# Kernel tuning notes

Measured on AMD Instinct MI355X. Metric: run time of the kernel, lower is better.

## Reference

```python
import jax, jax.numpy as jnp
import numpy as np

D_MODEL = 1024
NUM_HEADS = 16
D_K = D_MODEL // NUM_HEADS
B, L = 2, 2048


def setup_inputs() -> dict:
    key = jax.random.key(0)
    ks = jax.random.split(key, 10)
    s = 1.0 / np.sqrt(D_MODEL)
    inp = {
        "x": jax.random.normal(ks[0], (B, L, D_MODEL), dtype=jnp.float32),
        "mask": jnp.ones((B, L, L), dtype=jnp.int32),
        "wq": jax.random.uniform(ks[1], (D_MODEL, D_MODEL), jnp.float32, -s, s),
        "bq": jax.random.uniform(ks[2], (D_MODEL,), jnp.float32, -s, s),
        "wk": jax.random.uniform(ks[3], (D_MODEL, D_MODEL), jnp.float32, -s, s),
        "bk": jax.random.uniform(ks[4], (D_MODEL,), jnp.float32, -s, s),
        "wv": jax.random.uniform(ks[5], (D_MODEL, D_MODEL), jnp.float32, -s, s),
        "bv": jax.random.uniform(ks[6], (D_MODEL,), jnp.float32, -s, s),
        "wo": jax.random.uniform(ks[7], (D_MODEL, D_MODEL), jnp.float32, -s, s),
        "bo": jax.random.uniform(ks[8], (D_MODEL,), jnp.float32, -s, s),
    }
    return inp


def reference(x, mask, wq, bq, wk, bk, wv, bv, wo, bo):
    Bs, Ls, C = x.shape
    # linear projections, then split heads: [B, L, C] -> [B, h, L, d_k]
    def split_heads(t):
        return t.reshape(Bs, Ls, NUM_HEADS, D_K).transpose(0, 2, 1, 3)
    q = split_heads(x @ wq + bq)
    k = split_heads(x @ wk + bk)
    v = split_heads(x @ wv + bv)
    scores = jnp.einsum("bhlc,bhkc->bhlk", q, k) / np.sqrt(D_K)
    # mask: [B, L, L] -> [B, 1, L, L]; fill masked positions with -1e9
    scores = jnp.where(mask[:, None, :, :] == 0, jnp.float32(-1e9), scores)
    attn = jax.nn.softmax(scores, axis=-1)  # dropout p=0.0 -> identity
    out = jnp.einsum("bhlk,bhkc->bhlc", attn, v)
    out = out.transpose(0, 2, 1, 3).reshape(Bs, Ls, C)
    return out @ wo + bo
```

## Files before the change

kernel.cpp:

```cpp
#include <hip/hip_runtime.h>
#include <stdint.h>

#define D_MODEL 1024
#define NHEAD   16
#define DK      64
#define BATCH   2
#define SEQ     2048
#define MTOT    (BATCH*SEQ)

typedef unsigned short u16;
typedef unsigned int   u32;
typedef u16    u16x4  __attribute__((ext_vector_type(4)));
typedef u16    u16x8  __attribute__((ext_vector_type(8)));
typedef u32    u32x4  __attribute__((ext_vector_type(4)));
typedef __bf16 bf16x8 __attribute__((ext_vector_type(8)));
typedef float  f32x4  __attribute__((ext_vector_type(4)));
typedef float  f32x16 __attribute__((ext_vector_type(16)));

__device__ __forceinline__ u16 f2bf(float f) {
  union { float f; unsigned u; } v; v.f = f;
  return (u16)((v.u + 0x7fffu + ((v.u >> 16) & 1u)) >> 16);
}

__device__ __forceinline__ void gl_lds16(const void* g, void* l) {
  __builtin_amdgcn_global_load_lds((const __attribute__((address_space(1))) void*)g,
                                   (__attribute__((address_space(3))) void*)l, 16, 0, 0);
}

__device__ __forceinline__ bf16x8 ld_frag(const u16* p) {
  return __builtin_bit_cast(bf16x8, *(const u16x8*)p);
}

__device__ __forceinline__ u32 cvtpk(float lo, float hi) {
  u32 r;
  asm("v_cvt_pk_bf16_f32 %0, %1, %2" : "=v"(r) : "v"(lo), "v"(hi));
  return r;
}

__global__ __launch_bounds__(256) void k_prep(const float* __restrict__ x, u16* __restrict__ xb,
                                              const float* __restrict__ wq, const float* __restrict__ wk,
                                              const float* __restrict__ wv, const float* __restrict__ wo,
                                              u16* __restrict__ wqkv_t, u16* __restrict__ wo_t,
                                              const int* __restrict__ mask,
                                              unsigned long long* __restrict__ mb,
                                              u32* __restrict__ fullm) {
  const int bid = blockIdx.x;
  if (bid < 4096) {
    int i = bid * 256 + threadIdx.x;
    const float4 v = ((const float4*)x)[i];
    u16x4 o; o[0]=f2bf(v.x); o[1]=f2bf(v.y); o[2]=f2bf(v.z); o[3]=f2bf(v.w);
    *(u16x4*)(xb + (size_t)i*4) = o;
  } else if (bid < 8192) {
    __shared__ float tile[32][33];
    const int idx = bid - 4096;
    const int z = idx >> 10;
    const float* src = (z==0)?wq:(z==1)?wk:(z==2)?wv:wo;
    const int kb = ((idx >> 5) & 31)*32, nb = (idx & 31)*32;
    const int tx = threadIdx.x & 31, ty = threadIdx.x >> 5;
    #pragma unroll
    for (int i=0;i<4;i++)
      tile[ty + i*8][tx] = src[(size_t)(kb + ty + i*8)*D_MODEL + nb + tx];
    __syncthreads();
    u16* dst = (z<3) ? (wqkv_t + (size_t)z*D_MODEL*D_MODEL) : wo_t;
    #pragma unroll
    for (int i=0;i<4;i++) {
      int n = nb + ty + i*8, k = kb + tx;
      dst[(size_t)n*D_MODEL + k] = f2bf(tile[tx][ty + i*8]);
    }
  } else {
    const int wid = (bid - 8192)*4 + (threadIdx.x >> 6);
    const int lane = threadIdx.x & 63;
    u32 fmacc = 0;
    for (int t2 = 0; t2 < 32; ++t2) {
      int word = wid*32 + t2;
      int m = mask[(size_t)wid*SEQ + t2*64 + lane];
      unsigned long long bits = __ballot(m != 0);
      if (bits == ~0ull) fmacc |= (1u << t2);
      if (lane == 0) mb[word] = bits;
    }
    if (lane == 0) fullm[wid] = fmacc;
  }
}

__global__ __launch_bounds__(256) void k_vtrans(const u16* __restrict__ V, u16* __restrict__ Vt) {
  __shared__ u16 tile[64][72];
  const int bh = blockIdx.x >> 5;
  const int l0 = (blockIdx.x & 31) * 64;
  const int t = threadIdx.x;
  const u16* src = V + ((size_t)bh*SEQ + l0)*DK;
  #pragma unroll
  for (int j=0;j<2;j++) {
    int idx = t + j*256;
    int r = idx >> 3, c8 = (idx & 7)*8;
    *(u16x8*)&tile[r][c8] = *(const u16x8*)(src + (size_t)r*DK + c8);
  }
  __syncthreads();
  u16* dst = Vt + (size_t)bh*DK*SEQ + l0;
  #pragma unroll
  for (int j=0;j<2;j++) {
    int idx = t + j*256;
    int d = idx >> 3, k8 = (idx & 7)*8;
    u16x8 o;
    #pragma unroll
    for (int e=0;e<8;e++) o[e] = tile[k8 + e][d];
    *(u16x8*)(dst + (size_t)d*SEQ + k8) = o;
  }
}

template<int EPI>
__global__ __launch_bounds__(256) void k_gemm(const u16* __restrict__ A, const u16* __restrict__ Bt,
                                              const int M, const int N, const int K, const int nbm,
                                              const float* __restrict__ bq, const float* __restrict__ bk,
                                              const float* __restrict__ bv,
                                              u16* __restrict__ Qo, u16* __restrict__ Ko, u16* __restrict__ Vo,
                                              const float* __restrict__ bo, float* __restrict__ out) {
  __shared__ u16 As[2*128*32];
  __shared__ u16 Bs[2*128*32];
  const int t = threadIdx.x, lane = t & 63, w = t >> 6;
  const int cpx = gridDim.x >> 3;
  const int bswz = (blockIdx.x & 7)*cpx + (blockIdx.x >> 3);
  const int bm = bswz % nbm, bn = bswz / nbm;
  const int brow = bm*128, bcol = bn*128;

  const int srow = w*32 + (lane >> 2);
  const int sswz = (lane & 3) ^ ((lane >> 2) & 3);
  const u16* aS0 = A  + (size_t)(brow + srow)*K + sswz*8;
  const u16* aS1 = aS0 + (size_t)16*K;
  const u16* bS0 = Bt + (size_t)(bcol + srow)*K + sswz*8;
  const u16* bS1 = bS0 + (size_t)16*K;
  u16* aD = As + w*1024;
  u16* bD = Bs + w*1024;

  const int wr = w >> 1, wc = w & 1;
  const int slotA = (lane >> 4) ^ (lane & 3);
  const u16* aRd = As + (wr*64 + (lane & 15))*32 + slotA*8;
  const u16* bRd = Bs + (wc*64 + (lane & 15))*32 + slotA*8;

  f32x4 acc[4][4];
  #pragma unroll
  for (int i=0;i<4;i++)
    #pragma unroll
    for (int j=0;j<4;j++) acc[i][j] = (f32x4){0.f,0.f,0.f,0.f};

  gl_lds16(aS0, aD); gl_lds16(aS1, aD + 512);
  gl_lds16(bS0, bD); gl_lds16(bS1, bD + 512);
  asm volatile("s_waitcnt vmcnt(0)" ::: "memory");
  __builtin_amdgcn_s_barrier();

  int cur = 0;
  for (int kt = 0; kt < K; kt += 32, cur ^= 1) {
    if (kt + 32 < K) {
      const int nx = (cur ^ 1) * 4096;
      gl_lds16(aS0 + kt + 32, aD + nx); gl_lds16(aS1 + kt + 32, aD + nx + 512);
      gl_lds16(bS0 + kt + 32, bD + nx); gl_lds16(bS1 + kt + 32, bD + nx + 512);
    }
    const u16* aR = aRd + cur*4096;
    const u16* bR = bRd + cur*4096;
    bf16x8 af[4], bfr[4];
    #pragma unroll
    for (int m=0;m<4;m++) af[m] = ld_frag(aR + m*512);
    #pragma unroll
    for (int n=0;n<4;n++) bfr[n] = ld_frag(bR + n*512);
    #pragma unroll
    for (int m=0;m<4;m++)
      #pragma unroll
      for (int n=0;n<4;n++)
        acc[m][n] = __builtin_amdgcn_mfma_f32_16x16x32_bf16(af[m], bfr[n], acc[m][n], 0,0,0);
    asm volatile("s_waitcnt vmcnt(0) lgkmcnt(0)" ::: "memory");
    __builtin_amdgcn_s_barrier();
  }

  const int orow = brow + wr*64 + (lane >> 4)*4;
  const int ocol = bcol + wc*64 + (lane & 15);
  if (EPI == 0) {
    const int mat = ocol >> 10;
    const float* bias = (mat==0) ? bq : (mat==1) ? bk : bv;
    u16* outp = (mat==0) ? Qo : (mat==1) ? Ko : Vo;
    const float scal = (mat==0) ? 0.125f*1.4426950408889634f : 1.0f;
    #pragma unroll
    for (int m=0;m<4;m++) {
      #pragma unroll
      for (int n=0;n<4;n++) {
        int col = ocol + n*16;
        int c = col & 1023;
        float bb = bias[c];
        int h = c >> 6, d = c & 63;
        #pragma unroll
        for (int j=0;j<4;j++) {
          int row = orow + m*16 + j;
          int b = row >> 11, l = row & 2047;
          float v = (acc[m][n][j] + bb) * scal;
          outp[(((size_t)(b*NHEAD + h)*SEQ + l) << 6) + d] = f2bf(v);
        }
      }
    }
  } else {
    #pragma unroll
    for (int m=0;m<4;m++)
      #pragma unroll
      for (int n=0;n<4;n++) {
        int col = ocol + n*16;
        float bb = bo[col];
        #pragma unroll
        for (int j=0;j<4;j++) {
          int row = orow + m*16 + j;
          out[(size_t)row*N + col] = acc[m][n][j] + bb;
        }
      }
  }
}

__global__ __launch_bounds__(512, 4) void k_attn(const u16* __restrict__ Q, const u16* __restrict__ K,
                                                 const u16* __restrict__ Vt,
                                                 const unsigned long long* __restrict__ MB,
                                                 const u32* __restrict__ FM,
                                                 u16* __restrict__ AO) {
  __shared__ char smem[81920];
  const int t = threadIdx.x, lane = t & 63, w = t >> 6;
  const int hf = w >> 2, widx = w & 3;
  const int bid = blockIdx.x;
  const int swz = (bid & 7)*64 + (bid >> 3);
  const int bh = swz >> 4;
  const int q0 = (swz & 15) * 128;
  const int b = bh >> 4, h = bh & 15;
  const int lq = lane & 31, hi = lane >> 5, l7 = lane & 7;

  const int qg = q0 + widx*32 + lq;

  const int sswz = l7 ^ ((lane >> 3) & 7);
  const int srow = widx*16 + (lane >> 3);
  const u16* kSb = K  + ((size_t)bh*SEQ + srow)*DK + sswz*8;
  const u16* vSb = Vt + ((size_t)bh*DK + srow)*SEQ + sswz*8;

  u16* qlds = (u16*)(smem + 65536);
  {
    const int qsrow = w*16 + (lane >> 3);
    const u16* qS = Q + ((size_t)bh*SEQ + q0 + qsrow)*DK + sswz*8;
    gl_lds16(qS, qlds + w*1024);
    gl_lds16(qS + 8*DK, qlds + w*1024 + 512);
  }
  const u16* qrd = qlds + (widx*32 + lq)*64;

  const u32 fm = FM[(size_t)b*SEQ + qg];

  f32x16 o0 = 0.f, o1 = 0.f;
  float l_run = 0.f;

  #define STAGE(buf, tile) do {                                           \
    const u16* kp_ = kSb + (size_t)(tile)*64*DK;                          \
    const u16* vp_ = vSb + (size_t)(tile)*64;                             \
    u16* kd_ = (u16*)(smem + (buf)*32768 + hf*16384) + widx*1024;         \
    u16* vd_ = (u16*)(smem + (buf)*32768 + hf*16384 + 8192) + widx*1024;  \
    gl_lds16(kp_, kd_); gl_lds16(kp_ + 8*DK, kd_ + 512);                  \
    gl_lds16(vp_, vd_); gl_lds16(vp_ + 8*SEQ, vd_ + 512);                 \
  } while (0)

  STAGE(0, hf*16);
  asm volatile("s_waitcnt vmcnt(0)" ::: "memory");
  __builtin_amdgcn_s_barrier();

  for (int i = 0; i < 16; ++i) {
    const int cur = i & 1;
    if (i + 1 < 16) STAGE(cur ^ 1, hf*16 + i + 1);
    const u16* Kbuf = (const u16*)(smem + cur*32768 + hf*16384);
    const u16* Vbuf = (const u16*)(smem + cur*32768 + hf*16384 + 8192);
    const int ktg = hf*16 + i;
    const bool full = __all((fm >> ktg) & 1u);
    unsigned long long mb = ~0ull;
    if (!full) mb = MB[((size_t)b*SEQ + qg)*32 + ktg];

    #pragma unroll
    for (int sub = 0; sub < 2; ++sub) {
      f32x16 s = 0.f;
      __builtin_amdgcn_s_setprio(1);
      #pragma unroll
      for (int ks=0;ks<4;ks++) {
        const int ph = (ks*2 + hi) ^ l7;
        bf16x8 kf = ld_frag(Kbuf + (sub*32 + lq)*64 + ph*8);
        bf16x8 qf = ld_frag(qrd + ph*8);
        s = __builtin_amdgcn_mfma_f32_32x32x16_bf16(kf, qf, s, 0,0,0);
      }
      __builtin_amdgcn_s_setprio(0);

      if (!full) {
        #pragma unroll
        for (int r=0;r<16;r++) {
          int kl = sub*32 + (r&3) + 8*(r>>2) + 4*hi;
          if (!((mb >> kl) & 1ull)) s[r] = -1e9f;
        }
      }

      float ps;
      u32 w0, w1, w2, w3, w4, w5, w6, w7;
      {
        float e0 = __builtin_amdgcn_exp2f(s[0]);
        float e1 = __builtin_amdgcn_exp2f(s[1]);
        float e2 = __builtin_amdgcn_exp2f(s[2]);
        float e3 = __builtin_amdgcn_exp2f(s[3]);
        float e4 = __builtin_amdgcn_exp2f(s[4]);
        float e5 = __builtin_amdgcn_exp2f(s[5]);
        float e6 = __builtin_amdgcn_exp2f(s[6]);
        float e7 = __builtin_amdgcn_exp2f(s[7]);
        ps = ((e0+e1)+(e2+e3)) + ((e4+e5)+(e6+e7));
        w0 = cvtpk(e0, e1); w1 = cvtpk(e2, e3);
        w2 = cvtpk(e4, e5); w3 = cvtpk(e6, e7);
      }
      {
        float e0 = __builtin_amdgcn_exp2f(s[8]);
        float e1 = __builtin_amdgcn_exp2f(s[9]);
        float e2 = __builtin_amdgcn_exp2f(s[10]);
        float e3 = __builtin_amdgcn_exp2f(s[11]);
        float e4 = __builtin_amdgcn_exp2f(s[12]);
        float e5 = __builtin_amdgcn_exp2f(s[13]);
        float e6 = __builtin_amdgcn_exp2f(s[14]);
        float e7 = __builtin_amdgcn_exp2f(s[15]);
        ps += ((e0+e1)+(e2+e3)) + ((e4+e5)+(e6+e7));
        w4 = cvtpk(e0, e1); w5 = cvtpk(e2, e3);
        w6 = cvtpk(e4, e5); w7 = cvtpk(e6, e7);
      }
      l_run += ps;

      asm volatile("v_permlane32_swap_b32 %0, %1" : "+v"(w0), "+v"(w2));
      asm volatile("v_permlane32_swap_b32 %0, %1" : "+v"(w1), "+v"(w3));
      asm volatile("v_permlane32_swap_b32 %0, %1" : "+v"(w4), "+v"(w6));
      asm volatile("v_permlane32_swap_b32 %0, %1" : "+v"(w5), "+v"(w7));
      bf16x8 pa0 = __builtin_bit_cast(bf16x8, (u32x4){w0, w1, w2, w3});
      bf16x8 pa1 = __builtin_bit_cast(bf16x8, (u32x4){w4, w5, w6, w7});
      const int ph0 = ((sub*2+0)*2 + hi) ^ l7;
      const int ph1 = ((sub*2+1)*2 + hi) ^ l7;
      {
        bf16x8 v00 = ld_frag(Vbuf + lq*64 + ph0*8);
        bf16x8 v01 = ld_frag(Vbuf + lq*64 + ph1*8);
        __builtin_amdgcn_s_setprio(1);
        o0 = __builtin_amdgcn_mfma_f32_32x32x16_bf16(v00, pa0, o0, 0,0,0);
        o0 = __builtin_amdgcn_mfma_f32_32x32x16_bf16(v01, pa1, o0, 0,0,0);
        __builtin_amdgcn_s_setprio(0);
      }
      {
        bf16x8 v10 = ld_frag(Vbuf + (32+lq)*64 + ph0*8);
        bf16x8 v11 = ld_frag(Vbuf + (32+lq)*64 + ph1*8);
        __builtin_amdgcn_s_setprio(1);
        o1 = __builtin_amdgcn_mfma_f32_32x32x16_bf16(v10, pa0, o1, 0,0,0);
        o1 = __builtin_amdgcn_mfma_f32_32x32x16_bf16(v11, pa1, o1, 0,0,0);
        __builtin_amdgcn_s_setprio(0);
      }
    }

    asm volatile("s_waitcnt vmcnt(0) lgkmcnt(0)" ::: "memory");
    __builtin_amdgcn_s_barrier();
  }
  #undef STAGE

  l_run += __shfl_xor(l_run, 32);

  float* marea = (float*)smem;
  if (hf == 1) {
    float* p = marea + (size_t)(widx*64 + lane)*35;
    #pragma unroll
    for (int r=0;r<16;r++) { p[r] = o0[r]; p[16+r] = o1[r]; }
    p[32] = l_run;
  }
  __syncthreads();
  if (hf == 0) {
    const float* p = marea + (size_t)(widx*64 + lane)*35;
    float inv = 1.0f / (l_run + p[32]);
    size_t base = ((size_t)(b*SEQ + qg))*D_MODEL + h*DK;
    u16x4 g;
    #pragma unroll
    for (int rr=0;rr<4;rr++) {
      #pragma unroll
      for (int i2=0;i2<4;i2++) g[i2] = f2bf((o0[rr*4+i2] + p[rr*4+i2]) * inv);
      *(u16x4*)(AO + base + rr*8 + hi*4) = g;
    }
    #pragma unroll
    for (int rr=0;rr<4;rr++) {
      #pragma unroll
      for (int i2=0;i2<4;i2++) g[i2] = f2bf((o1[rr*4+i2] + p[16+rr*4+i2]) * inv);
      *(u16x4*)(AO + base + 32 + rr*8 + hi*4) = g;
    }
  }
}

extern "C" void kernel_launch(void* const* d_in, const int* in_sizes, int n_in,
                              void* d_out, int out_size, void* d_ws, size_t ws_size,
                              hipStream_t stream) {
  const float* x  = (const float*)d_in[0];
  const int*  msk = (const int*)d_in[1];
  const float* wq = (const float*)d_in[2];
  const float* bq = (const float*)d_in[3];
  const float* wk = (const float*)d_in[4];
  const float* bk = (const float*)d_in[5];
  const float* wv = (const float*)d_in[6];
  const float* bv = (const float*)d_in[7];
  const float* wo = (const float*)d_in[8];
  const float* bo = (const float*)d_in[9];
  float* out = (float*)d_out;

  char* ws = (char*)d_ws;
  size_t off = 0;
  u16* Xb   = (u16*)(ws + off); off += (size_t)MTOT*D_MODEL*2;
  u16* Wqkv = (u16*)(ws + off); off += (size_t)3*D_MODEL*D_MODEL*2;
  u16* Wot  = (u16*)(ws + off); off += (size_t)D_MODEL*D_MODEL*2;
  u16* Qb   = (u16*)(ws + off); off += (size_t)BATCH*NHEAD*SEQ*DK*2;
  u16* Kb   = (u16*)(ws + off); off += (size_t)BATCH*NHEAD*SEQ*DK*2;
  u16* Vb   = (u16*)(ws + off); off += (size_t)BATCH*NHEAD*SEQ*DK*2;
  u16* Vtb  = (u16*)(ws + off); off += (size_t)BATCH*NHEAD*SEQ*DK*2;
  u16* AO   = (u16*)(ws + off); off += (size_t)MTOT*D_MODEL*2;
  unsigned long long* Mb = (unsigned long long*)(ws + off); off += (size_t)MTOT*32*8;
  u32* FM   = (u32*)(ws + off); off += (size_t)MTOT*4;

  k_prep<<<9216, 256, 0, stream>>>(x, Xb, wq, wk, wv, wo, Wqkv, Wot, msk, Mb, FM);
  k_gemm<0><<<(MTOT/128)*(3*D_MODEL/128), 256, 0, stream>>>(
      Xb, Wqkv, MTOT, 3*D_MODEL, D_MODEL, MTOT/128,
      bq, bk, bv, Qb, Kb, Vb, nullptr, nullptr);
  k_vtrans<<<BATCH*NHEAD*(SEQ/64), 256, 0, stream>>>(Vb, Vtb);
  k_attn<<<BATCH*NHEAD*(SEQ/128), 512, 0, stream>>>(Qb, Kb, Vtb, Mb, FM, AO);
  k_gemm<1><<<(MTOT/128)*(D_MODEL/128), 256, 0, stream>>>(
      AO, Wot, MTOT, D_MODEL, D_MODEL, MTOT/128,
      nullptr, nullptr, nullptr, nullptr, nullptr, nullptr, bo, out);
}
```

Before: 133.8 us.

## Fuse V transpose into QKV GEMM epilogue and triple-buffer GEMM staging

Removes the separate V transpose kernel by having the QKV GEMM write V tiles directly in transposed [B,H,D,L] layout, staging the tile through shared memory for coalesced stores. The GEMM main loop moves from double to triple buffering with a prefetch distance of two, waiting with vmcnt(4) so global loads overlap more compute. This saves one kernel launch and a full V round-trip through memory. In exchange it uses more LDS per block (48KB), which may lower occupancy.

```diff
diff --git a/kernel.cpp b/kernel.cpp
--- a/kernel.cpp
+++ b/kernel.cpp
@@ -82,31 +82,6 @@
   }
 }
 
-__global__ __launch_bounds__(256) void k_vtrans(const u16* __restrict__ V, u16* __restrict__ Vt) {
-  __shared__ u16 tile[64][72];
-  const int bh = blockIdx.x >> 5;
-  const int l0 = (blockIdx.x & 31) * 64;
-  const int t = threadIdx.x;
-  const u16* src = V + ((size_t)bh*SEQ + l0)*DK;
-  #pragma unroll
-  for (int j=0;j<2;j++) {
-    int idx = t + j*256;
-    int r = idx >> 3, c8 = (idx & 7)*8;
-    *(u16x8*)&tile[r][c8] = *(const u16x8*)(src + (size_t)r*DK + c8);
-  }
-  __syncthreads();
-  u16* dst = Vt + (size_t)bh*DK*SEQ + l0;
-  #pragma unroll
-  for (int j=0;j<2;j++) {
-    int idx = t + j*256;
-    int d = idx >> 3, k8 = (idx & 7)*8;
-    u16x8 o;
-    #pragma unroll
-    for (int e=0;e<8;e++) o[e] = tile[k8 + e][d];
-    *(u16x8*)(dst + (size_t)d*SEQ + k8) = o;
-  }
-}
-
 template<int EPI>
 __global__ __launch_bounds__(256) void k_gemm(const u16* __restrict__ A, const u16* __restrict__ Bt,
                                               const int M, const int N, const int K, const int nbm,
@@ -114,8 +89,7 @@
                                               const float* __restrict__ bv,
                                               u16* __restrict__ Qo, u16* __restrict__ Ko, u16* __restrict__ Vo,
                                               const float* __restrict__ bo, float* __restrict__ out) {
-  __shared__ u16 As[2*128*32];
-  __shared__ u16 Bs[2*128*32];
+  __shared__ char smem[49152];
   const int t = threadIdx.x, lane = t & 63, w = t >> 6;
   const int cpx = gridDim.x >> 3;
   const int bswz = (blockIdx.x & 7)*cpx + (blockIdx.x >> 3);
@@ -128,13 +102,11 @@
   const u16* aS1 = aS0 + (size_t)16*K;
   const u16* bS0 = Bt + (size_t)(bcol + srow)*K + sswz*8;
   const u16* bS1 = bS0 + (size_t)16*K;
-  u16* aD = As + w*1024;
-  u16* bD = Bs + w*1024;
 
   const int wr = w >> 1, wc = w & 1;
   const int slotA = (lane >> 4) ^ (lane & 3);
-  const u16* aRd = As + (wr*64 + (lane & 15))*32 + slotA*8;
-  const u16* bRd = Bs + (wc*64 + (lane & 15))*32 + slotA*8;
+  const int aOff = (wr*64 + (lane & 15))*32 + slotA*8;
+  const int bOff = (wc*64 + (lane & 15))*32 + slotA*8;
 
   f32x4 acc[4][4];
   #pragma unroll
@@ -142,20 +114,25 @@
     #pragma unroll
     for (int j=0;j<4;j++) acc[i][j] = (f32x4){0.f,0.f,0.f,0.f};
 
-  gl_lds16(aS0, aD); gl_lds16(aS1, aD + 512);
-  gl_lds16(bS0, bD); gl_lds16(bS1, bD + 512);
-  asm volatile("s_waitcnt vmcnt(0)" ::: "memory");
+  #define GSTAGE(buf, kt0) do {                                        \
+    u16* ad_ = (u16*)(smem + (buf)*16384) + w*1024;                    \
+    u16* bd_ = (u16*)(smem + (buf)*16384 + 8192) + w*1024;             \
+    gl_lds16(aS0 + (kt0), ad_); gl_lds16(aS1 + (kt0), ad_ + 512);      \
+    gl_lds16(bS0 + (kt0), bd_); gl_lds16(bS1 + (kt0), bd_ + 512);      \
+  } while (0)
+
+  const int NT = K >> 5;
+  GSTAGE(0, 0);
+  GSTAGE(1, 32);
+  asm volatile("s_waitcnt vmcnt(4)" ::: "memory");
   __builtin_amdgcn_s_barrier();
 
-  int cur = 0;
-  for (int kt = 0; kt < K; kt += 32, cur ^= 1) {
-    if (kt + 32 < K) {
-      const int nx = (cur ^ 1) * 4096;
-      gl_lds16(aS0 + kt + 32, aD + nx); gl_lds16(aS1 + kt + 32, aD + nx + 512);
-      gl_lds16(bS0 + kt + 32, bD + nx); gl_lds16(bS1 + kt + 32, bD + nx + 512);
-    }
-    const u16* aR = aRd + cur*4096;
-    const u16* bR = bRd + cur*4096;
+  int cur = 0, nx = 2;
+  for (int it = 0; it < NT; ++it) {
+    const bool more = (it + 2 < NT);
+    if (more) GSTAGE(nx, (it + 2) << 5);
+    const u16* aR = (const u16*)(smem + cur*16384) + aOff;
+    const u16* bR = (const u16*)(smem + cur*16384 + 8192) + bOff;
     bf16x8 af[4], bfr[4];
     #pragma unroll
     for (int m=0;m<4;m++) af[m] = ld_frag(aR + m*512);
@@ -166,31 +143,63 @@
       #pragma unroll
       for (int n=0;n<4;n++)
         acc[m][n] = __builtin_amdgcn_mfma_f32_16x16x32_bf16(af[m], bfr[n], acc[m][n], 0,0,0);
-    asm volatile("s_waitcnt vmcnt(0) lgkmcnt(0)" ::: "memory");
+    if (more) asm volatile("s_waitcnt vmcnt(4) lgkmcnt(0)" ::: "memory");
+    else      asm volatile("s_waitcnt vmcnt(0) lgkmcnt(0)" ::: "memory");
     __builtin_amdgcn_s_barrier();
-  }
+    cur = (cur == 2) ? 0 : cur + 1;
+    nx  = (nx  == 2) ? 0 : nx  + 1;
+  }
+  #undef GSTAGE
 
   const int orow = brow + wr*64 + (lane >> 4)*4;
   const int ocol = bcol + wc*64 + (lane & 15);
   if (EPI == 0) {
     const int mat = ocol >> 10;
-    const float* bias = (mat==0) ? bq : (mat==1) ? bk : bv;
-    u16* outp = (mat==0) ? Qo : (mat==1) ? Ko : Vo;
-    const float scal = (mat==0) ? 0.125f*1.4426950408889634f : 1.0f;
-    #pragma unroll
-    for (int m=0;m<4;m++) {
+    if (mat == 2) {
+      __syncthreads();
+      u16* tb = (u16*)smem;
       #pragma unroll
       for (int n=0;n<4;n++) {
-        int col = ocol + n*16;
-        int c = col & 1023;
-        float bb = bias[c];
-        int h = c >> 6, d = c & 63;
+        const int c_local = wc*64 + (lane & 15) + n*16;
+        const float bb = bv[(ocol + n*16) & 1023];
         #pragma unroll
-        for (int j=0;j<4;j++) {
-          int row = orow + m*16 + j;
-          int b = row >> 11, l = row & 2047;
-          float v = (acc[m][n][j] + bb) * scal;
-          outp[(((size_t)(b*NHEAD + h)*SEQ + l) << 6) + d] = f2bf(v);
+        for (int m=0;m<4;m++) {
+          const int l0 = wr*64 + (lane >> 4)*4 + m*16;
+          u16x4 g;
+          #pragma unroll
+          for (int j=0;j<4;j++) g[j] = f2bf(acc[m][n][j] + bb);
+          *(u16x4*)&tb[c_local*132 + l0] = g;
+        }
+      }
+      __syncthreads();
+      const int r = t >> 1, half = t & 1;
+      const int cfull = (bcol + r) & 1023;
+      const int b = brow >> 11, h = cfull >> 6, d = cfull & 63;
+      const int lbase = (brow & 2047) + half*64;
+      u16* dst = Vo + ((size_t)((b*NHEAD + h)*DK + d))*SEQ + lbase;
+      const u16* srcl = &tb[r*132 + half*64];
+      #pragma unroll
+      for (int s=0;s<8;s++)
+        *(u16x8*)(dst + s*8) = *(const u16x8*)(srcl + s*8);
+    } else {
+      const float* bias = (mat==0) ? bq : bk;
+      u16* outp = (mat==0) ? Qo : Ko;
+      const float scal = (mat==0) ? 0.125f*1.4426950408889634f : 1.0f;
+      #pragma unroll
+      for (int m=0;m<4;m++) {
+        #pragma unroll
+        for (int n=0;n<4;n++) {
+          int col = ocol + n*16;
+          int c = col & 1023;
+          float bb = bias[c];
+          int h = c >> 6, d = c & 63;
+          #pragma unroll
+          for (int j=0;j<4;j++) {
+            int row = orow + m*16 + j;
+            int b = row >> 11, l = row & 2047;
+            float v = (acc[m][n][j] + bb) * scal;
+            outp[(((size_t)(b*NHEAD + h)*SEQ + l) << 6) + d] = f2bf(v);
+          }
         }
       }
     }
@@ -403,7 +412,6 @@
   u16* Wot  = (u16*)(ws + off); off += (size_t)D_MODEL*D_MODEL*2;
   u16* Qb   = (u16*)(ws + off); off += (size_t)BATCH*NHEAD*SEQ*DK*2;
   u16* Kb   = (u16*)(ws + off); off += (size_t)BATCH*NHEAD*SEQ*DK*2;
-  u16* Vb   = (u16*)(ws + off); off += (size_t)BATCH*NHEAD*SEQ*DK*2;
   u16* Vtb  = (u16*)(ws + off); off += (size_t)BATCH*NHEAD*SEQ*DK*2;
   u16* AO   = (u16*)(ws + off); off += (size_t)MTOT*D_MODEL*2;
   unsigned long long* Mb = (unsigned long long*)(ws + off); off += (size_t)MTOT*32*8;
@@ -412,8 +420,7 @@
   k_prep<<<9216, 256, 0, stream>>>(x, Xb, wq, wk, wv, wo, Wqkv, Wot, msk, Mb, FM);
   k_gemm<0><<<(MTOT/128)*(3*D_MODEL/128), 256, 0, stream>>>(
       Xb, Wqkv, MTOT, 3*D_MODEL, D_MODEL, MTOT/128,
-      bq, bk, bv, Qb, Kb, Vb, nullptr, nullptr);
-  k_vtrans<<<BATCH*NHEAD*(SEQ/64), 256, 0, stream>>>(Vb, Vtb);
+      bq, bk, bv, Qb, Kb, Vtb, nullptr, nullptr);
   k_attn<<<BATCH*NHEAD*(SEQ/128), 512, 0, stream>>>(Qb, Kb, Vtb, Mb, FM, AO);
   k_gemm<1><<<(MTOT/128)*(D_MODEL/128), 256, 0, stream>>>(
       AO, Wot, MTOT, D_MODEL, D_MODEL, MTOT/128,
```

Result: no change. 132.1 us (-1.3%).
